# Kernel optimization log

Hardware: AMD Instinct MI355X
Metric: run time of the kernel (lower is better)

Reference implementation:

```python
import jax, jax.numpy as jnp
import numpy as np

NUM_NODES = 2048
NUM_FEATURES = 512
NUM_CLASSES = 128
INF = 1e9  # finite stand-in for float('inf'): identical shortest-path results on
           # connected positive-weight graphs, but keeps gradients NaN-free


def bellman_ford(adj_matrix, source_node):
    """Min-plus Bellman-Ford relaxation.

    Returns:
      distances:    (N, N) where distances[v, i] = shortest dist source->v using <= i edges
      predecessors: (N,)   argmin predecessor on the final relaxation
      has_negative_cycle: () bool, True if an N-th relaxation still improves
    """
    n = adj_matrix.shape[0]
    init = jnp.full((n,), INF, dtype=adj_matrix.dtype).at[source_node].set(0.0)

    def step(dist, _):
        # new[v] = min(dist[v], min_u dist[u] + w(u, v))  -- one relaxation sweep
        new = jnp.minimum(dist, jnp.min(dist[:, None] + adj_matrix, axis=0))
        return new, new

    step = jax.checkpoint(step)  # O(N) saved state per step instead of O(N^2)
    final, hist = jax.lax.scan(step, init, None, length=n - 1)

    distances = jnp.concatenate([init[:, None], hist.T], axis=1)  # (N, N)

    relax = jnp.min(final[:, None] + adj_matrix, axis=0)
    predecessors = jnp.where(relax <= final,
                             jnp.argmin(final[:, None] + adj_matrix, axis=0),
                             -1)
    has_negative_cycle = jnp.any(jnp.minimum(final, relax) < final)
    return distances, predecessors, has_negative_cycle


def setup_inputs() -> dict:
    key = jax.random.key(0)
    k1, k2, k3 = jax.random.split(key, 3)
    adj_matrix = jax.random.uniform(k1, (NUM_NODES, NUM_NODES), dtype=jnp.float32)
    node_embedding = jax.random.normal(k2, (NUM_NODES, NUM_FEATURES), dtype=jnp.float32)
    fc_weight = jax.random.normal(k3, (NUM_CLASSES, NUM_FEATURES + NUM_NODES), dtype=jnp.float32) * 0.02
    fc_bias = jnp.zeros((NUM_CLASSES,), dtype=jnp.float32)
    return {
        "adj_matrix": adj_matrix,
        "node_embedding": node_embedding,
        "fc_weight": fc_weight,
        "fc_bias": fc_bias,
        "source_node": 0,
    }


def reference(adj_matrix, node_embedding, fc_weight, fc_bias, source_node):
    distances, predecessors, has_negative_cycle = bellman_ford(adj_matrix, source_node)
    # node_embedding plays the role of Embedding(arange(N)) lookup = full table
    node_features = jnp.concatenate([node_embedding, distances], axis=1)  # (N, F+N)
    output = node_features @ fc_weight.T + fc_bias  # (N, C)
    return output, has_negative_cycle
```

## Files before the change

### kernel.cpp

```cpp
#include <hip/hip_runtime.h>

#define NN   2048
#define FF   512
#define CC   128
#define WROW 2560
#define INFV 1.0e9f
#define NB   128
#define NT   1024
#define BN   16
#define MAGIC 0xB00F5EEDu

#define AL32(p)   __hip_atomic_load((p),  __ATOMIC_RELAXED, __HIP_MEMORY_SCOPE_AGENT)
#define AS32(p,v) __hip_atomic_store((p), (v), __ATOMIC_RELAXED, __HIP_MEMORY_SCOPE_AGENT)
#define AL64(p)   __hip_atomic_load((p),  __ATOMIC_RELAXED, __HIP_MEMORY_SCOPE_AGENT)
#define AS64(p,v) __hip_atomic_store((p), (v), __ATOMIC_RELAXED, __HIP_MEMORY_SCOPE_AGENT)

struct WS {
    unsigned long long D64[2][NN / 2];
    unsigned T[2][NB][16];
    unsigned long long Suf[CC][8];
};

__device__ __forceinline__ unsigned long long pk(unsigned tag, float v) {
    return ((unsigned long long)tag << 32) | (unsigned long long)__float_as_uint(v);
}
__device__ __forceinline__ unsigned tg(unsigned long long e) { return (unsigned)(e >> 32); }
__device__ __forceinline__ float    vl(unsigned long long e) { return __uint_as_float((unsigned)e); }

__global__ __launch_bounds__(NT, 1)
void bf_nosync(const float* __restrict__ adj,
               const float* __restrict__ emb,
               const float* __restrict__ W,
               const float* __restrict__ bias,
               const int*   __restrict__ srcp,
               float*       __restrict__ out,
               WS* ws, int out_size)
{
    __shared__ __align__(16) float adjT[BN * NN];
    __shared__ __align__(16) float dist[NN];
    __shared__ float    wcol[CC];
    __shared__ float    red16[16];
    __shared__ unsigned redc[16];

    const int tid = threadIdx.x;
    const int b   = blockIdx.x;
    const int src = *srcp;
    const int q   = (b & 7) * 16 + (b >> 3);
    const int vb  = q * BN;

    if (tid == 0) AS32(&ws->T[1][b][0], MAGIC);
    if (tid < BN)
        AS32(((unsigned*)&ws->D64[0][0]) + (vb + tid),
             __float_as_uint(((vb + tid) == src) ? 0.0f : INFV));
    if (tid < 64) asm volatile("s_waitcnt vmcnt(0)" ::: "memory");
    if (tid == 0) AS32(&ws->T[0][b][0], MAGIC);

    #pragma unroll
    for (int it = 0; it < 8; ++it) {
        int r = tid + NT * it;
        int u = r >> 2, qc = (r & 3) * 4;
        float4 a = *(const float4*)(adj + (size_t)u * NN + vb + qc);
        adjT[(qc + 0) * NN + u] = a.x;
        adjT[(qc + 1) * NN + u] = a.y;
        adjT[(qc + 2) * NN + u] = a.z;
        adjT[(qc + 3) * NN + u] = a.w;
    }
    dist[tid]      = (tid == src) ? 0.0f : INFV;
    dist[tid + NT] = ((tid + NT) == src) ? 0.0f : INFV;
    __syncthreads();

    const int vown = tid >> 6;
    const int lane = tid & 63;
    const int c0 = 2 * lane, c1 = c0 + 1;
    const int vE = vb + (tid & 15);
    const int cE = (2 * (tid >> 4)) & 127;
    float ea0 = 0.0f, ea1 = 0.0f;
    float dprev_r = ((vb + vown) == src) ? 0.0f : INFV;

    float acc0, acc1;
    { float d0 = dprev_r;
      acc0 = d0 * W[(size_t)c0 * WROW + FF];
      acc1 = d0 * W[(size_t)c1 * WROW + FF]; }

    int kconv = -1, hneg = 0;

    for (int s = 1; s <= NN; ++s) {
        const int p = (s - 1) & 1;
        if (tid < NB) {
            const unsigned want = (s == 1) ? MAGIC : (unsigned)(s - 1);
            unsigned f = AL32(&ws->T[p][tid][0]);
            while (f != want) { __builtin_amdgcn_s_sleep(1); f = AL32(&ws->T[p][tid][0]); }
        }
        __syncthreads();
        if (s < NN && vown == 1) {
            wcol[lane]      = W[(size_t)lane * WROW + FF + s];
            wcol[64 + lane] = W[(size_t)(64 + lane) * WROW + FF + s];
        }
        {
            unsigned long long e = AL64(&ws->D64[p][tid]);
            float n0 = __uint_as_float((unsigned)e);
            float n1 = __uint_as_float((unsigned)(e >> 32));
            unsigned ch = (n0 != dist[2 * tid]) | (n1 != dist[2 * tid + 1]);
            dist[2 * tid] = n0; dist[2 * tid + 1] = n1;
            unsigned long long bal = __ballot(ch != 0);
            if (lane == 0) redc[vown] = (bal != 0ull) ? 1u : 0u;
        }
        __syncthreads();
        unsigned any = 0;
        #pragma unroll
        for (int w = 0; w < 16; ++w) any |= redc[w];
        if (s >= 2 && !any) { kconv = s - 1; break; }

        if (s - 1 < 16) {
            int i0 = 32 * (s - 1);
            const float4* ep = (const float4*)(emb + (size_t)vE * FF + i0);
            const float4* wa = (const float4*)(W + (size_t)cE * WROW + i0);
            const float4* wb = (const float4*)(W + (size_t)(cE + 1) * WROW + i0);
            #pragma unroll
            for (int j = 0; j < 8; ++j) {
                float4 e = ep[j], x = wa[j], y = wb[j];
                ea0 += e.x*x.x + e.y*x.y + e.z*x.z + e.w*x.w;
                ea1 += e.x*y.x + e.y*y.y + e.z*y.z + e.w*y.w;
            }
        }

        float m = 4.0e9f;
        const float* ar = adjT + vown * NN;
        #pragma unroll
        for (int k = 0; k < 8; ++k) {
            int u = 4 * lane + 256 * k;
            float4 dd = *(const float4*)(dist + u);
            float4 aa = *(const float4*)(ar + u);
            m = fminf(m, fminf(fminf(dd.x + aa.x, dd.y + aa.y),
                               fminf(dd.z + aa.z, dd.w + aa.w)));
        }
        #pragma unroll
        for (int st = 1; st < 64; st <<= 1) m = fminf(m, __shfl_xor(m, st, 64));
        float nv = fminf(dprev_r, m);
        dprev_r = nv;

        if (lane == 0)
            AS32(((unsigned*)&ws->D64[s & 1][0]) + (vb + vown), __float_as_uint(nv));
        asm volatile("s_waitcnt vmcnt(0)" ::: "memory");
        __syncthreads();
        if (tid == 0) AS32(&ws->T[s & 1][b][0], (unsigned)s);

        if (s < NN) {
            acc0 = fmaf(nv, wcol[c0], acc0);
            acc1 = fmaf(nv, wcol[c1], acc1);
        }
    }

    if (kconv < 0) {
        if (tid < NB) {
            unsigned f = AL32(&ws->T[0][tid][0]);
            while (f != (unsigned)NN) { __builtin_amdgcn_s_sleep(1); f = AL32(&ws->T[0][tid][0]); }
        }
        __syncthreads();
        unsigned long long e = AL64(&ws->D64[0][tid]);
        unsigned ch = (__uint_as_float((unsigned)e) != dist[2 * tid]) |
                      (__uint_as_float((unsigned)(e >> 32)) != dist[2 * tid + 1]);
        unsigned long long bal = __ballot(ch != 0);
        if (lane == 0) redc[vown] = (bal != 0ull) ? 1u : 0u;
        __syncthreads();
        unsigned any = 0;
        #pragma unroll
        for (int w = 0; w < 16; ++w) any |= redc[w];
        hneg = any ? 1 : 0;
    } else if (kconv >= 1 && kconv <= NN - 2) {
        float ssum = 0.0f;
        for (int i = kconv + 1 + tid; i <= NN - 1; i += NT)
            ssum += W[(size_t)b * WROW + FF + i];
        #pragma unroll
        for (int st = 1; st < 64; st <<= 1) ssum += __shfl_xor(ssum, st, 64);
        if (lane == 0) red16[vown] = ssum;
        __syncthreads();
        if (tid == 0) {
            float x = 0.0f;
            #pragma unroll
            for (int w = 0; w < 16; ++w) x += red16[w];
            AS64(&ws->Suf[b][0], pk(0x40000000u + (unsigned)kconv, x));
        }
        const unsigned wantS = 0x40000000u + (unsigned)kconv;
        unsigned long long s0 = AL64(&ws->Suf[c0][0]);
        while (tg(s0) != wantS) { __builtin_amdgcn_s_sleep(1); s0 = AL64(&ws->Suf[c0][0]); }
        unsigned long long s1 = AL64(&ws->Suf[c1][0]);
        while (tg(s1) != wantS) { __builtin_amdgcn_s_sleep(1); s1 = AL64(&ws->Suf[c1][0]); }
        float dv = dist[vb + vown];
        acc0 = fmaf(dv, vl(s0), acc0);
        acc1 = fmaf(dv, vl(s1), acc1);
    }

    for (int chk = (kconv < 0 ? 16 : (kconv < 16 ? kconv : 16)); chk < 16; ++chk) {
        int i0 = 32 * chk;
        const float4* ep = (const float4*)(emb + (size_t)vE * FF + i0);
        const float4* wa = (const float4*)(W + (size_t)cE * WROW + i0);
        const float4* wb = (const float4*)(W + (size_t)(cE + 1) * WROW + i0);
        #pragma unroll
        for (int j = 0; j < 8; ++j) {
            float4 e = ep[j], x = wa[j], y = wb[j];
            ea0 += e.x*x.x + e.y*x.y + e.z*x.z + e.w*x.w;
            ea1 += e.x*y.x + e.y*y.y + e.z*y.z + e.w*y.w;
        }
    }

    __syncthreads();
    float* comb = adjT;
    comb[(tid & 15) * 129 + cE]     = ea0;
    comb[(tid & 15) * 129 + cE + 1] = ea1;
    __syncthreads();
    float o0 = acc0 + comb[vown * 129 + c0] + bias[c0];
    float o1 = acc1 + comb[vown * 129 + c1] + bias[c1];
    *(float2*)(out + (size_t)(vb + vown) * CC + c0) = make_float2(o0, o1);
    if (b == 0 && tid == 0 && out_size > NN * CC)
        out[NN * CC] = hneg ? 1.0f : 0.0f;
}

extern "C" void kernel_launch(void* const* d_in, const int* in_sizes, int n_in,
                              void* d_out, int out_size, void* d_ws, size_t ws_size,
                              hipStream_t stream) {
    const float* adj  = (const float*)d_in[0];
    const float* emb  = (const float*)d_in[1];
    const float* W    = (const float*)d_in[2];
    const float* bias = (const float*)d_in[3];
    const int*   srcp = (const int*)d_in[4];
    float* outp = (float*)d_out;
    WS* ws = (WS*)d_ws;
    int osz = out_size;

    bf_nosync<<<dim3(NB), dim3(NT), 0, stream>>>(adj, emb, W, bias, srcp,
                                                 outp, ws, osz);
}
```

Baseline: 142.9 us.

## Replace per-block step flags with tagged distance entries and defer FC work

Drops the separate per-block flag array. Each distance value is now published as a 64-bit word holding the step number and the value, so readers spin on the data itself instead of on a flag followed by a data load. This removes one store, the vmcnt wait and one barrier per relaxation step. The per-step loading of W columns into shared memory and the embedding dot products are moved out of the loop: the first HCAP steps are kept in a shared history buffer and folded into the output after convergence. The cost is twice the bytes per distance entry and more polling loads per thread, since every thread now spins on two global words each step.

```diff
diff --git a/kernel.cpp b/kernel.cpp
--- a/kernel.cpp
+++ b/kernel.cpp
@@ -8,16 +8,13 @@
 #define NB   128
 #define NT   1024
 #define BN   16
-#define MAGIC 0xB00F5EEDu
+#define HCAP 96
 
-#define AL32(p)   __hip_atomic_load((p),  __ATOMIC_RELAXED, __HIP_MEMORY_SCOPE_AGENT)
-#define AS32(p,v) __hip_atomic_store((p), (v), __ATOMIC_RELAXED, __HIP_MEMORY_SCOPE_AGENT)
 #define AL64(p)   __hip_atomic_load((p),  __ATOMIC_RELAXED, __HIP_MEMORY_SCOPE_AGENT)
 #define AS64(p,v) __hip_atomic_store((p), (v), __ATOMIC_RELAXED, __HIP_MEMORY_SCOPE_AGENT)
 
 struct WS {
-    unsigned long long D64[2][NN / 2];
-    unsigned T[2][NB][16];
+    unsigned long long D[2][NN];
     unsigned long long Suf[CC][8];
 };
 
@@ -28,19 +25,18 @@
 __device__ __forceinline__ float    vl(unsigned long long e) { return __uint_as_float((unsigned)e); }
 
 __global__ __launch_bounds__(NT, 1)
-void bf_nosync(const float* __restrict__ adj,
-               const float* __restrict__ emb,
-               const float* __restrict__ W,
-               const float* __restrict__ bias,
-               const int*   __restrict__ srcp,
-               float*       __restrict__ out,
-               WS* ws, int out_size)
+void bf_lean(const float* __restrict__ adj,
+             const float* __restrict__ emb,
+             const float* __restrict__ W,
+             const float* __restrict__ bias,
+             const int*   __restrict__ srcp,
+             float*       __restrict__ out,
+             WS* ws, int out_size)
 {
     __shared__ __align__(16) float adjT[BN * NN];
     __shared__ __align__(16) float dist[NN];
-    __shared__ float    wcol[CC];
-    __shared__ float    red16[16];
-    __shared__ unsigned redc[16];
+    __shared__ float hist[HCAP][BN];
+    __shared__ float red16[BN];
 
     const int tid = threadIdx.x;
     const int b   = blockIdx.x;
@@ -48,12 +44,8 @@
     const int q   = (b & 7) * 16 + (b >> 3);
     const int vb  = q * BN;
 
-    if (tid == 0) AS32(&ws->T[1][b][0], MAGIC);
     if (tid < BN)
-        AS32(((unsigned*)&ws->D64[0][0]) + (vb + tid),
-             __float_as_uint(((vb + tid) == src) ? 0.0f : INFV));
-    if (tid < 64) asm volatile("s_waitcnt vmcnt(0)" ::: "memory");
-    if (tid == 0) AS32(&ws->T[0][b][0], MAGIC);
+        AS64(&ws->D[0][vb + tid], pk(0u, ((vb + tid) == src) ? 0.0f : INFV));
 
     #pragma unroll
     for (int it = 0; it < 8; ++it) {
@@ -65,64 +57,34 @@
         adjT[(qc + 2) * NN + u] = a.z;
         adjT[(qc + 3) * NN + u] = a.w;
     }
-    dist[tid]      = (tid == src) ? 0.0f : INFV;
-    dist[tid + NT] = ((tid + NT) == src) ? 0.0f : INFV;
     __syncthreads();
 
     const int vown = tid >> 6;
     const int lane = tid & 63;
     const int c0 = 2 * lane, c1 = c0 + 1;
-    const int vE = vb + (tid & 15);
-    const int cE = (2 * (tid >> 4)) & 127;
-    float ea0 = 0.0f, ea1 = 0.0f;
-    float dprev_r = ((vb + vown) == src) ? 0.0f : INFV;
+    float p0 = (tid == src) ? 0.0f : INFV;
+    float p1 = ((tid + NT) == src) ? 0.0f : INFV;
 
     float acc0, acc1;
-    { float d0 = dprev_r;
+    { float d0 = ((vb + vown) == src) ? 0.0f : INFV;
       acc0 = d0 * W[(size_t)c0 * WROW + FF];
       acc1 = d0 * W[(size_t)c1 * WROW + FF]; }
 
     int kconv = -1, hneg = 0;
 
     for (int s = 1; s <= NN; ++s) {
-        const int p = (s - 1) & 1;
-        if (tid < NB) {
-            const unsigned want = (s == 1) ? MAGIC : (unsigned)(s - 1);
-            unsigned f = AL32(&ws->T[p][tid][0]);
-            while (f != want) { __builtin_amdgcn_s_sleep(1); f = AL32(&ws->T[p][tid][0]); }
-        }
-        __syncthreads();
-        if (s < NN && vown == 1) {
-            wcol[lane]      = W[(size_t)lane * WROW + FF + s];
-            wcol[64 + lane] = W[(size_t)(64 + lane) * WROW + FF + s];
-        }
-        {
-            unsigned long long e = AL64(&ws->D64[p][tid]);
-            float n0 = __uint_as_float((unsigned)e);
-            float n1 = __uint_as_float((unsigned)(e >> 32));
-            unsigned ch = (n0 != dist[2 * tid]) | (n1 != dist[2 * tid + 1]);
-            dist[2 * tid] = n0; dist[2 * tid + 1] = n1;
-            unsigned long long bal = __ballot(ch != 0);
-            if (lane == 0) redc[vown] = (bal != 0ull) ? 1u : 0u;
-        }
-        __syncthreads();
-        unsigned any = 0;
-        #pragma unroll
-        for (int w = 0; w < 16; ++w) any |= redc[w];
+        const int pp = (s - 1) & 1;
+        const unsigned want = (unsigned)(s - 1);
+        unsigned long long e0 = AL64(&ws->D[pp][tid]);
+        while (tg(e0) != want) { __builtin_amdgcn_s_sleep(1); e0 = AL64(&ws->D[pp][tid]); }
+        unsigned long long e1 = AL64(&ws->D[pp][tid + NT]);
+        while (tg(e1) != want) { __builtin_amdgcn_s_sleep(1); e1 = AL64(&ws->D[pp][tid + NT]); }
+        float n0 = vl(e0), n1 = vl(e1);
+        int ch = (n0 != p0) | (n1 != p1);
+        p0 = n0; p1 = n1;
+        dist[tid] = n0; dist[tid + NT] = n1;
+        int any = __syncthreads_or(ch);
         if (s >= 2 && !any) { kconv = s - 1; break; }
-
-        if (s - 1 < 16) {
-            int i0 = 32 * (s - 1);
-            const float4* ep = (const float4*)(emb + (size_t)vE * FF + i0);
-            const float4* wa = (const float4*)(W + (size_t)cE * WROW + i0);
-            const float4* wb = (const float4*)(W + (size_t)(cE + 1) * WROW + i0);
-            #pragma unroll
-            for (int j = 0; j < 8; ++j) {
-                float4 e = ep[j], x = wa[j], y = wb[j];
-                ea0 += e.x*x.x + e.y*x.y + e.z*x.z + e.w*x.w;
-                ea1 += e.x*y.x + e.y*y.y + e.z*y.z + e.w*y.w;
-            }
-        }
 
         float m = 4.0e9f;
         const float* ar = adjT + vown * NN;
@@ -136,37 +98,26 @@
         }
         #pragma unroll
         for (int st = 1; st < 64; st <<= 1) m = fminf(m, __shfl_xor(m, st, 64));
-        float nv = fminf(dprev_r, m);
-        dprev_r = nv;
+        float nv = fminf(dist[vb + vown], m);
 
-        if (lane == 0)
-            AS32(((unsigned*)&ws->D64[s & 1][0]) + (vb + vown), __float_as_uint(nv));
-        asm volatile("s_waitcnt vmcnt(0)" ::: "memory");
+        if (lane == 0) {
+            AS64(&ws->D[s & 1][vb + vown], pk((unsigned)s, nv));
+            if (s <= HCAP) hist[s - 1][vown] = nv;
+        }
+        if (s > HCAP && s < NN) {
+            acc0 = fmaf(nv, W[(size_t)c0 * WROW + FF + s], acc0);
+            acc1 = fmaf(nv, W[(size_t)c1 * WROW + FF + s], acc1);
+        }
         __syncthreads();
-        if (tid == 0) AS32(&ws->T[s & 1][b][0], (unsigned)s);
-
-        if (s < NN) {
-            acc0 = fmaf(nv, wcol[c0], acc0);
-            acc1 = fmaf(nv, wcol[c1], acc1);
-        }
     }
 
     if (kconv < 0) {
-        if (tid < NB) {
-            unsigned f = AL32(&ws->T[0][tid][0]);
-            while (f != (unsigned)NN) { __builtin_amdgcn_s_sleep(1); f = AL32(&ws->T[0][tid][0]); }
-        }
-        __syncthreads();
-        unsigned long long e = AL64(&ws->D64[0][tid]);
-        unsigned ch = (__uint_as_float((unsigned)e) != dist[2 * tid]) |
-                      (__uint_as_float((unsigned)(e >> 32)) != dist[2 * tid + 1]);
-        unsigned long long bal = __ballot(ch != 0);
-        if (lane == 0) redc[vown] = (bal != 0ull) ? 1u : 0u;
-        __syncthreads();
-        unsigned any = 0;
-        #pragma unroll
-        for (int w = 0; w < 16; ++w) any |= redc[w];
-        hneg = any ? 1 : 0;
+        unsigned long long e0 = AL64(&ws->D[0][tid]);
+        while (tg(e0) != (unsigned)NN) { __builtin_amdgcn_s_sleep(1); e0 = AL64(&ws->D[0][tid]); }
+        unsigned long long e1 = AL64(&ws->D[0][tid + NT]);
+        while (tg(e1) != (unsigned)NN) { __builtin_amdgcn_s_sleep(1); e1 = AL64(&ws->D[0][tid + NT]); }
+        int ch = (vl(e0) != p0) | (vl(e1) != p1);
+        hneg = __syncthreads_or(ch) ? 1 : 0;
     } else if (kconv >= 1 && kconv <= NN - 2) {
         float ssum = 0.0f;
         for (int i = kconv + 1 + tid; i <= NN - 1; i += NT)
@@ -178,7 +129,7 @@
         if (tid == 0) {
             float x = 0.0f;
             #pragma unroll
-            for (int w = 0; w < 16; ++w) x += red16[w];
+            for (int w = 0; w < BN; ++w) x += red16[w];
             AS64(&ws->Suf[b][0], pk(0x40000000u + (unsigned)kconv, x));
         }
         const unsigned wantS = 0x40000000u + (unsigned)kconv;
@@ -191,7 +142,20 @@
         acc1 = fmaf(dv, vl(s1), acc1);
     }
 
-    for (int chk = (kconv < 0 ? 16 : (kconv < 16 ? kconv : 16)); chk < 16; ++chk) {
+    {
+        int fmax = (kconv < 0) ? (NN - 1) : kconv;
+        if (fmax > HCAP) fmax = HCAP;
+        for (int s2 = 1; s2 <= fmax; ++s2) {
+            float dv = hist[s2 - 1][vown];
+            acc0 = fmaf(dv, W[(size_t)c0 * WROW + FF + s2], acc0);
+            acc1 = fmaf(dv, W[(size_t)c1 * WROW + FF + s2], acc1);
+        }
+    }
+
+    const int vE = vb + (tid & 15);
+    const int cE = (2 * (tid >> 4)) & 127;
+    float ea0 = 0.0f, ea1 = 0.0f;
+    for (int chk = 0; chk < 16; ++chk) {
         int i0 = 32 * chk;
         const float4* ep = (const float4*)(emb + (size_t)vE * FF + i0);
         const float4* wa = (const float4*)(W + (size_t)cE * WROW + i0);
@@ -228,6 +192,6 @@
     WS* ws = (WS*)d_ws;
     int osz = out_size;
 
-    bf_nosync<<<dim3(NB), dim3(NT), 0, stream>>>(adj, emb, W, bias, srcp,
-                                                 outp, ws, osz);
+    bf_lean<<<dim3(NB), dim3(NT), 0, stream>>>(adj, emb, W, bias, srcp,
+                                               outp, ws, osz);
 }
```

Result: slower. 151.2 us (+5.9%).

## Compute first two relaxations locally and prefetch W columns to skip grid barriers

Applied to the files above, without the earlier changes.

Each block initialises its dist from the source row of adj, so after step 1 the distances are known without a grid exchange. It then computes step 2 locally, which removes the magic-tag handshake and the first two cross-block barrier rounds. The embedding GEMV is hoisted out of the relaxation loop into one pass. The W distance columns for the first 40 steps are preloaded into shared memory instead of being fetched each step. This relies on the graph converging within a few iterations for the per-step W preload to matter, and it adds shared memory use.

```diff
diff --git a/kernel.cpp b/kernel.cpp
--- a/kernel.cpp
+++ b/kernel.cpp
@@ -8,52 +8,41 @@
 #define NB   128
 #define NT   1024
 #define BN   16
-#define MAGIC 0xB00F5EEDu
+#define WPATS 40
 
 #define AL32(p)   __hip_atomic_load((p),  __ATOMIC_RELAXED, __HIP_MEMORY_SCOPE_AGENT)
 #define AS32(p,v) __hip_atomic_store((p), (v), __ATOMIC_RELAXED, __HIP_MEMORY_SCOPE_AGENT)
 #define AL64(p)   __hip_atomic_load((p),  __ATOMIC_RELAXED, __HIP_MEMORY_SCOPE_AGENT)
 #define AS64(p,v) __hip_atomic_store((p), (v), __ATOMIC_RELAXED, __HIP_MEMORY_SCOPE_AGENT)
 
+typedef unsigned long long ull;
+
 struct WS {
-    unsigned long long D64[2][NN / 2];
+    ull      D64[2][NN / 2];
     unsigned T[2][NB][16];
-    unsigned long long Suf[CC][8];
+    ull      Suf[CC][8];
 };
 
-__device__ __forceinline__ unsigned long long pk(unsigned tag, float v) {
-    return ((unsigned long long)tag << 32) | (unsigned long long)__float_as_uint(v);
-}
-__device__ __forceinline__ unsigned tg(unsigned long long e) { return (unsigned)(e >> 32); }
-__device__ __forceinline__ float    vl(unsigned long long e) { return __uint_as_float((unsigned)e); }
-
 __global__ __launch_bounds__(NT, 1)
-void bf_nosync(const float* __restrict__ adj,
-               const float* __restrict__ emb,
-               const float* __restrict__ W,
-               const float* __restrict__ bias,
-               const int*   __restrict__ srcp,
-               float*       __restrict__ out,
-               WS* ws, int out_size)
+void bf_fast(const float* __restrict__ adj,
+             const float* __restrict__ emb,
+             const float* __restrict__ W,
+             const float* __restrict__ bias,
+             const int*   __restrict__ srcp,
+             float*       __restrict__ out,
+             WS* ws, int out_size)
 {
     __shared__ __align__(16) float adjT[BN * NN];
     __shared__ __align__(16) float dist[NN];
-    __shared__ float    wcol[CC];
-    __shared__ float    red16[16];
-    __shared__ unsigned redc[16];
+    __shared__ float    wpat[WPATS][CC];
+    __shared__ float    red16[BN];
+    __shared__ unsigned redc[BN];
 
     const int tid = threadIdx.x;
     const int b   = blockIdx.x;
     const int src = *srcp;
     const int q   = (b & 7) * 16 + (b >> 3);
     const int vb  = q * BN;
-
-    if (tid == 0) AS32(&ws->T[1][b][0], MAGIC);
-    if (tid < BN)
-        AS32(((unsigned*)&ws->D64[0][0]) + (vb + tid),
-             __float_as_uint(((vb + tid) == src) ? 0.0f : INFV));
-    if (tid < 64) asm volatile("s_waitcnt vmcnt(0)" ::: "memory");
-    if (tid == 0) AS32(&ws->T[0][b][0], MAGIC);
 
     #pragma unroll
     for (int it = 0; it < 8; ++it) {
@@ -65,65 +54,16 @@
         adjT[(qc + 2) * NN + u] = a.z;
         adjT[(qc + 3) * NN + u] = a.w;
     }
-    dist[tid]      = (tid == src) ? 0.0f : INFV;
-    dist[tid + NT] = ((tid + NT) == src) ? 0.0f : INFV;
+    dist[tid]      = (tid == src) ? 0.0f : adj[(size_t)src * NN + tid];
+    dist[tid + NT] = ((tid + NT) == src) ? 0.0f : adj[(size_t)src * NN + tid + NT];
     __syncthreads();
 
     const int vown = tid >> 6;
     const int lane = tid & 63;
     const int c0 = 2 * lane, c1 = c0 + 1;
-    const int vE = vb + (tid & 15);
-    const int cE = (2 * (tid >> 4)) & 127;
-    float ea0 = 0.0f, ea1 = 0.0f;
-    float dprev_r = ((vb + vown) == src) ? 0.0f : INFV;
-
-    float acc0, acc1;
-    { float d0 = dprev_r;
-      acc0 = d0 * W[(size_t)c0 * WROW + FF];
-      acc1 = d0 * W[(size_t)c1 * WROW + FF]; }
-
-    int kconv = -1, hneg = 0;
-
-    for (int s = 1; s <= NN; ++s) {
-        const int p = (s - 1) & 1;
-        if (tid < NB) {
-            const unsigned want = (s == 1) ? MAGIC : (unsigned)(s - 1);
-            unsigned f = AL32(&ws->T[p][tid][0]);
-            while (f != want) { __builtin_amdgcn_s_sleep(1); f = AL32(&ws->T[p][tid][0]); }
-        }
-        __syncthreads();
-        if (s < NN && vown == 1) {
-            wcol[lane]      = W[(size_t)lane * WROW + FF + s];
-            wcol[64 + lane] = W[(size_t)(64 + lane) * WROW + FF + s];
-        }
-        {
-            unsigned long long e = AL64(&ws->D64[p][tid]);
-            float n0 = __uint_as_float((unsigned)e);
-            float n1 = __uint_as_float((unsigned)(e >> 32));
-            unsigned ch = (n0 != dist[2 * tid]) | (n1 != dist[2 * tid + 1]);
-            dist[2 * tid] = n0; dist[2 * tid + 1] = n1;
-            unsigned long long bal = __ballot(ch != 0);
-            if (lane == 0) redc[vown] = (bal != 0ull) ? 1u : 0u;
-        }
-        __syncthreads();
-        unsigned any = 0;
-        #pragma unroll
-        for (int w = 0; w < 16; ++w) any |= redc[w];
-        if (s >= 2 && !any) { kconv = s - 1; break; }
-
-        if (s - 1 < 16) {
-            int i0 = 32 * (s - 1);
-            const float4* ep = (const float4*)(emb + (size_t)vE * FF + i0);
-            const float4* wa = (const float4*)(W + (size_t)cE * WROW + i0);
-            const float4* wb = (const float4*)(W + (size_t)(cE + 1) * WROW + i0);
-            #pragma unroll
-            for (int j = 0; j < 8; ++j) {
-                float4 e = ep[j], x = wa[j], y = wb[j];
-                ea0 += e.x*x.x + e.y*x.y + e.z*x.z + e.w*x.w;
-                ea1 += e.x*y.x + e.y*y.y + e.z*y.z + e.w*y.w;
-            }
-        }
-
+
+    float nv2;
+    {
         float m = 4.0e9f;
         const float* ar = adjT + vown * NN;
         #pragma unroll
@@ -136,8 +76,83 @@
         }
         #pragma unroll
         for (int st = 1; st < 64; st <<= 1) m = fminf(m, __shfl_xor(m, st, 64));
-        float nv = fminf(dprev_r, m);
-        dprev_r = nv;
+        nv2 = fminf(dist[vb + vown], m);
+    }
+
+    if (lane == 0)
+        AS32(((unsigned*)&ws->D64[0][0]) + (vb + vown), __float_as_uint(nv2));
+    asm volatile("s_waitcnt vmcnt(0)" ::: "memory");
+    __syncthreads();
+    if (tid == 0) AS32(&ws->T[0][b][0], 2u);
+
+    float acc0, acc1;
+    {
+        float d0 = ((vb + vown) == src) ? 0.0f : INFV;
+        float d1 = dist[vb + vown];
+        acc0 = d0 * W[(size_t)c0 * WROW + FF];
+        acc1 = d0 * W[(size_t)c1 * WROW + FF];
+        acc0 = fmaf(d1, W[(size_t)c0 * WROW + FF + 1], acc0);
+        acc1 = fmaf(d1, W[(size_t)c1 * WROW + FF + 1], acc1);
+        acc0 = fmaf(nv2, W[(size_t)c0 * WROW + FF + 2], acc0);
+        acc1 = fmaf(nv2, W[(size_t)c1 * WROW + FF + 2], acc1);
+    }
+    for (int r = tid; r < CC * WPATS; r += NT) {
+        int c = r / WPATS, j = r - c * WPATS;
+        wpat[j][c] = W[(size_t)c * WROW + FF + 1 + j];
+    }
+    const int vE = vb + (tid & 15);
+    const int cE = (2 * (tid >> 4)) & 127;
+    float ea0 = 0.0f, ea1 = 0.0f;
+    {
+        const float4* ep = (const float4*)(emb + (size_t)vE * FF);
+        const float4* wa = (const float4*)(W + (size_t)cE * WROW);
+        const float4* wb = (const float4*)(W + (size_t)(cE + 1) * WROW);
+        #pragma unroll 4
+        for (int j = 0; j < FF / 4; ++j) {
+            float4 e = ep[j], x = wa[j], y = wb[j];
+            ea0 += e.x*x.x + e.y*x.y + e.z*x.z + e.w*x.w;
+            ea1 += e.x*y.x + e.y*y.y + e.z*y.z + e.w*y.w;
+        }
+    }
+
+    int kconv = -1, hneg = 0;
+
+    for (int s = 3; s <= NN; ++s) {
+        const int p = (s - 1) & 1;
+        if (tid < NB) {
+            const unsigned want = (unsigned)(s - 1);
+            unsigned f = AL32(&ws->T[p][tid][0]);
+            while (f != want) { __builtin_amdgcn_s_sleep(1); f = AL32(&ws->T[p][tid][0]); }
+        }
+        __syncthreads();
+        {
+            ull e = AL64(&ws->D64[p][tid]);
+            float n0 = __uint_as_float((unsigned)e);
+            float n1 = __uint_as_float((unsigned)(e >> 32));
+            unsigned ch = (n0 != dist[2 * tid]) | (n1 != dist[2 * tid + 1]);
+            dist[2 * tid] = n0; dist[2 * tid + 1] = n1;
+            ull bal = __ballot(ch != 0);
+            if (lane == 0) redc[vown] = (bal != 0ull) ? 1u : 0u;
+        }
+        __syncthreads();
+        unsigned any = 0;
+        #pragma unroll
+        for (int w = 0; w < BN; ++w) any |= redc[w];
+        if (!any) { kconv = s - 1; break; }
+
+        float m = 4.0e9f;
+        const float* ar = adjT + vown * NN;
+        #pragma unroll
+        for (int k = 0; k < 8; ++k) {
+            int u = 4 * lane + 256 * k;
+            float4 dd = *(const float4*)(dist + u);
+            float4 aa = *(const float4*)(ar + u);
+            m = fminf(m, fminf(fminf(dd.x + aa.x, dd.y + aa.y),
+                               fminf(dd.z + aa.z, dd.w + aa.w)));
+        }
+        #pragma unroll
+        for (int st = 1; st < 64; st <<= 1) m = fminf(m, __shfl_xor(m, st, 64));
+        float nv = fminf(dist[vb + vown], m);
 
         if (lane == 0)
             AS32(((unsigned*)&ws->D64[s & 1][0]) + (vb + vown), __float_as_uint(nv));
@@ -146,8 +161,11 @@
         if (tid == 0) AS32(&ws->T[s & 1][b][0], (unsigned)s);
 
         if (s < NN) {
-            acc0 = fmaf(nv, wcol[c0], acc0);
-            acc1 = fmaf(nv, wcol[c1], acc1);
+            float w0, w1;
+            if (s <= WPATS) { w0 = wpat[s - 1][c0]; w1 = wpat[s - 1][c1]; }
+            else { w0 = W[(size_t)c0 * WROW + FF + s]; w1 = W[(size_t)c1 * WROW + FF + s]; }
+            acc0 = fmaf(nv, w0, acc0);
+            acc1 = fmaf(nv, w1, acc1);
         }
     }
 
@@ -157,17 +175,17 @@
             while (f != (unsigned)NN) { __builtin_amdgcn_s_sleep(1); f = AL32(&ws->T[0][tid][0]); }
         }
         __syncthreads();
-        unsigned long long e = AL64(&ws->D64[0][tid]);
+        ull e = AL64(&ws->D64[0][tid]);
         unsigned ch = (__uint_as_float((unsigned)e) != dist[2 * tid]) |
                       (__uint_as_float((unsigned)(e >> 32)) != dist[2 * tid + 1]);
-        unsigned long long bal = __ballot(ch != 0);
+        ull bal = __ballot(ch != 0);
         if (lane == 0) redc[vown] = (bal != 0ull) ? 1u : 0u;
         __syncthreads();
         unsigned any = 0;
         #pragma unroll
-        for (int w = 0; w < 16; ++w) any |= redc[w];
+        for (int w = 0; w < BN; ++w) any |= redc[w];
         hneg = any ? 1 : 0;
-    } else if (kconv >= 1 && kconv <= NN - 2) {
+    } else if (kconv >= 2 && kconv <= NN - 2) {
         float ssum = 0.0f;
         for (int i = kconv + 1 + tid; i <= NN - 1; i += NT)
             ssum += W[(size_t)b * WROW + FF + i];
@@ -178,30 +196,19 @@
         if (tid == 0) {
             float x = 0.0f;
             #pragma unroll
-            for (int w = 0; w < 16; ++w) x += red16[w];
-            AS64(&ws->Suf[b][0], pk(0x40000000u + (unsigned)kconv, x));
+            for (int w = 0; w < BN; ++w) x += red16[w];
+            AS64(&ws->Suf[b][0],
+                 ((ull)(0x40000000u + (unsigned)kconv) << 32) |
+                 (ull)__float_as_uint(x));
         }
         const unsigned wantS = 0x40000000u + (unsigned)kconv;
-        unsigned long long s0 = AL64(&ws->Suf[c0][0]);
-        while (tg(s0) != wantS) { __builtin_amdgcn_s_sleep(1); s0 = AL64(&ws->Suf[c0][0]); }
-        unsigned long long s1 = AL64(&ws->Suf[c1][0]);
-        while (tg(s1) != wantS) { __builtin_amdgcn_s_sleep(1); s1 = AL64(&ws->Suf[c1][0]); }
+        ull s0 = AL64(&ws->Suf[c0][0]);
+        while ((unsigned)(s0 >> 32) != wantS) { __builtin_amdgcn_s_sleep(1); s0 = AL64(&ws->Suf[c0][0]); }
+        ull s1 = AL64(&ws->Suf[c1][0]);
+        while ((unsigned)(s1 >> 32) != wantS) { __builtin_amdgcn_s_sleep(1); s1 = AL64(&ws->Suf[c1][0]); }
         float dv = dist[vb + vown];
-        acc0 = fmaf(dv, vl(s0), acc0);
-        acc1 = fmaf(dv, vl(s1), acc1);
-    }
-
-    for (int chk = (kconv < 0 ? 16 : (kconv < 16 ? kconv : 16)); chk < 16; ++chk) {
-        int i0 = 32 * chk;
-        const float4* ep = (const float4*)(emb + (size_t)vE * FF + i0);
-        const float4* wa = (const float4*)(W + (size_t)cE * WROW + i0);
-        const float4* wb = (const float4*)(W + (size_t)(cE + 1) * WROW + i0);
-        #pragma unroll
-        for (int j = 0; j < 8; ++j) {
-            float4 e = ep[j], x = wa[j], y = wb[j];
-            ea0 += e.x*x.x + e.y*x.y + e.z*x.z + e.w*x.w;
-            ea1 += e.x*y.x + e.y*y.y + e.z*y.z + e.w*y.w;
-        }
+        acc0 = fmaf(dv, __uint_as_float((unsigned)s0), acc0);
+        acc1 = fmaf(dv, __uint_as_float((unsigned)s1), acc1);
     }
 
     __syncthreads();
@@ -228,6 +235,6 @@
     WS* ws = (WS*)d_ws;
     int osz = out_size;
 
-    bf_nosync<<<dim3(NB), dim3(NT), 0, stream>>>(adj, emb, W, bias, srcp,
-                                                 outp, ws, osz);
+    bf_fast<<<dim3(NB), dim3(NT), 0, stream>>>(adj, emb, W, bias, srcp,
+                                               outp, ws, osz);
 }
```

Measured after the change: 146.5 us. 1.03x slower.
